# Performance work log

Hardware: AMD Instinct MI355X
Metric: run time of the kernel (lower is better)

## Reference

```python
import jax, jax.numpy as jnp
import numpy as np

EPS = 1e-12  # torch F.normalize eps


def _normalize(x):
    n = jnp.sqrt(jnp.sum(x * x, axis=1, keepdims=True))
    return x / jnp.maximum(n, EPS)


def _exp_sim(a, b, temp):
    # exp(a @ b.T / temp); returns (diag [B], row_sum [B,1])
    m = jnp.exp(jnp.matmul(a, b.T) / temp)
    return jnp.diagonal(m), jnp.sum(m, axis=1, keepdims=True)


def reference(x):
    temp = 0.1
    bsz = x.shape[0] // 3
    xn = _normalize(x)
    xe, ye, ze = xn[:bsz], xn[bsz:2 * bsz], xn[2 * bsz:]

    d_xx, s_xx = _exp_sim(xe, xe, temp)
    d_yy, s_yy = _exp_sim(ye, ye, temp)
    d_xy, s_xy = _exp_sim(xe, ye, temp)
    d_ax, s_ax = _exp_sim(xe, ze, temp)
    d_ay, s_ay = _exp_sim(ye, ze, temp)
    d_zx, s_zx = _exp_sim(ze, xe, temp)
    d_zy, s_zy = _exp_sim(ze, ye, temp)

    # NOTE: diag terms are [B], row-sums are [B,1] -> denominator broadcasts to
    # [B,B], matching the original torch broadcasting exactly.
    denom_mutual = (s_xy - d_xy) + (s_xx - d_xx) + (s_yy - d_yy)  # [B,B]
    loss_mutual = jnp.mean(-2.0 * jnp.log(d_xy / denom_mutual))

    def aux(d, s):
        return jnp.mean(-jnp.log(d / (s - d)))  # d/[B,B] -> [B,B]

    loss = (loss_mutual + aux(d_ax, s_ax) + aux(d_ay, s_ay)
            + aux(d_zx, s_zx) + aux(d_zy, s_zy))
    return loss


def setup_inputs() -> dict:
    key = jax.random.key(0)
    x = jax.random.normal(key, (12288, 128), dtype=jnp.float32)
    return {"x": x}
```

## Files before the change

### kernel.cpp

```cpp
#include <hip/hip_runtime.h>
#include <hip/hip_bf16.h>


typedef __attribute__((ext_vector_type(8))) short short8;
typedef __attribute__((ext_vector_type(4))) float floatx4;

#define D      128
#define BM     128
#define BN     64
#define BPAD   136
#define JSPLIT 32
#define NTPB   2
#define GRID_EXPSIM (5 * 32 * 32)

__global__ __launch_bounds__(256) void normalize_kernel(
    const float* __restrict__ x, short* __restrict__ xn,
    float* __restrict__ out, int rows) {
  int tid = threadIdx.x;
  if (blockIdx.x == 0 && tid == 0) out[0] = 0.0f;

  int row  = blockIdx.x * 4 + (tid >> 6);
  int lane = tid & 63;
  if (row >= rows) return;
  const float2* xr = (const float2*)(x + (size_t)row * D);
  float2 v = xr[lane];
  float s = v.x * v.x + v.y * v.y;
#pragma unroll
  for (int off = 1; off < 64; off <<= 1) s += __shfl_xor(s, off, 64);
  float scale = 3.7982825470322528f / fmaxf(sqrtf(s), 1e-12f);
  __hip_bfloat162 h;
  h.x = __float2bfloat16(v.x * scale);
  h.y = __float2bfloat16(v.y * scale);
  ((__hip_bfloat162*)xn)[(size_t)row * 64 + lane] = h;
}

template <bool COL, bool DIAG>
__device__ __forceinline__ void epilogue(
    const floatx4 (&acc)[2][4], float (&rs)[2][4], int rowg0, int colg0,
    int quad, int lm, int w, int t, float* __restrict__ csLDS,
    float* __restrict__ diag_ptr) {
  float cs[4] = {0.f, 0.f, 0.f, 0.f};
#pragma unroll
  for (int mi = 0; mi < 2; mi++) {
#pragma unroll
    for (int r = 0; r < 4; r++) {
      int rowg = rowg0 + mi * 16 + quad * 4 + r;
      float part = 0.f;
#pragma unroll
      for (int ni = 0; ni < 4; ni++) {
        float e = exp2f(acc[mi][ni][r]);
        part += e;
        if (COL) cs[ni] += e;
        if (DIAG) {
          if (colg0 + ni * 16 + lm == rowg) diag_ptr[rowg] = e;
        }
      }
      rs[mi][r] += part;
    }
  }
  if (COL) {
#pragma unroll
    for (int ni = 0; ni < 4; ni++) {
      float v = cs[ni];
      v += __shfl_xor(v, 16, 64);
      v += __shfl_xor(v, 32, 64);
      if (quad == 0) csLDS[w * 128 + t * 64 + ni * 16 + lm] = v;
    }
  }
}

__global__ __launch_bounds__(256) void expsim_kernel(
    const short* __restrict__ xn,
    float* __restrict__ srow,
    float* __restrict__ scol,
    float* __restrict__ diag,
    int bsz) {
  __shared__ short ldsB[BN * BPAD];
  __shared__ float csLDS[4 * 128];

  int tid = threadIdx.x;
  int bx  = blockIdx.x;
  int task   = bx >> 10;
  int rem    = bx & 1023;
  int iblk   = rem >> 5;
  int jsplit = rem & 31;

  const int aoff_t[5] = {0, 1, 0, 0, 1};
  const int boff_t[5] = {0, 1, 1, 2, 2};
  int arow0     = aoff_t[task] * bsz + iblk * BM;
  int brow_base = boff_t[task] * bsz;
  bool col_en   = (task >= 3);
  bool dg       = (jsplit == iblk);

  int w    = tid >> 6;
  int lane = tid & 63;
  int quad = lane >> 4;
  int lm   = lane & 15;
  int rowg0 = iblk * BM + w * 32;

  float* diag_ptr = diag + task * bsz;

  short8 afrag[2][4];
#pragma unroll
  for (int mi = 0; mi < 2; mi++) {
    int r = arow0 + w * 32 + mi * 16 + lm;
    const short8* ap = (const short8*)(xn + (size_t)r * D);
#pragma unroll
    for (int kk = 0; kk < 4; kk++) afrag[mi][kk] = ap[kk * 4 + quad];
  }

  float rs[2][4];
#pragma unroll
  for (int mi = 0; mi < 2; mi++)
#pragma unroll
    for (int r = 0; r < 4; r++) rs[mi][r] = 0.0f;

  const floatx4 z4 = {0.f, 0.f, 0.f, 0.f};

  for (int t = 0; t < NTPB; t++) {
    int jt    = jsplit * NTPB + t;
    int colg0 = jt * BN;
    __syncthreads();
    const short* bsrc = xn + ((size_t)brow_base + colg0) * D;
#pragma unroll
    for (int it = 0; it < 4; it++) {
      int c = it * 256 + tid;
      int br = c >> 4, c16 = c & 15;
      *(short8*)(&ldsB[br * BPAD + c16 * 8]) =
          *(const short8*)(bsrc + (size_t)br * D + c16 * 8);
    }
    __syncthreads();

    floatx4 acc[2][4];
#pragma unroll
    for (int kk = 0; kk < 4; kk++) {
      short8 bfrag[4];
#pragma unroll
      for (int ni = 0; ni < 4; ni++)
        bfrag[ni] = *(const short8*)(&ldsB[(ni * 16 + lm) * BPAD + kk * 32 + quad * 8]);
#pragma unroll
      for (int mi = 0; mi < 2; mi++)
#pragma unroll
        for (int ni = 0; ni < 4; ni++)
          acc[mi][ni] = __builtin_amdgcn_mfma_f32_16x16x32_bf16(
              afrag[mi][kk], bfrag[ni], (kk == 0) ? z4 : acc[mi][ni], 0, 0, 0);
    }

    if (col_en) {
      if (dg) epilogue<true, true>(acc, rs, rowg0, colg0, quad, lm, w, t, csLDS, diag_ptr);
      else    epilogue<true, false>(acc, rs, rowg0, colg0, quad, lm, w, t, csLDS, diag_ptr);
    } else {
      if (dg) epilogue<false, true>(acc, rs, rowg0, colg0, quad, lm, w, t, csLDS, diag_ptr);
      else    epilogue<false, false>(acc, rs, rowg0, colg0, quad, lm, w, t, csLDS, diag_ptr);
    }
  }

  float* srow_ptr = srow + ((size_t)(task * JSPLIT + jsplit)) * bsz;
#pragma unroll
  for (int mi = 0; mi < 2; mi++) {
#pragma unroll
    for (int r = 0; r < 4; r++) {
      float v = rs[mi][r];
      v += __shfl_xor(v, 1, 64);
      v += __shfl_xor(v, 2, 64);
      v += __shfl_xor(v, 4, 64);
      v += __shfl_xor(v, 8, 64);
      if (lm == 0) srow_ptr[rowg0 + mi * 16 + quad * 4 + r] = v;
    }
  }

  if (col_en) {
    __syncthreads();
    float* scol_ptr = scol + ((size_t)((task - 3) * 32 + iblk)) * bsz + jsplit * 128;
    if (tid < 128)
      scol_ptr[tid] = csLDS[tid] + csLDS[128 + tid] + csLDS[256 + tid] + csLDS[384 + tid];
  }
}

__global__ __launch_bounds__(256) void reduce_kernel(
    const float* __restrict__ srow, const float* __restrict__ scol,
    const float* __restrict__ diag, float* __restrict__ out, int bsz) {
  int tid = threadIdx.x;
  int i   = blockIdx.x * 256 + tid;

  float s[5];
#pragma unroll
  for (int t = 0; t < 5; t++) {
    float a = 0.f;
#pragma unroll 8
    for (int js = 0; js < JSPLIT; js++) a += srow[(size_t)(t * JSPLIT + js) * bsz + i];
    s[t] = a;
  }
  float s_zx = 0.f, s_zy = 0.f;
#pragma unroll 8
  for (int ib = 0; ib < 32; ib++) {
    s_zx += scol[(size_t)ib * bsz + i];
    s_zy += scol[(size_t)(32 + ib) * bsz + i];
  }
  float d_xx = diag[0 * bsz + i], d_yy = diag[1 * bsz + i];
  float d_xy = diag[2 * bsz + i], d_ax = diag[3 * bsz + i];
  float d_ay = diag[4 * bsz + i];

  float denom = (s[2] - d_xy) + (s[0] - d_xx) + (s[1] - d_yy);
  float tloc = -2.0f * __logf(d_xy / denom);
  tloc -= __logf(d_ax / (s[3] - d_ax));
  tloc -= __logf(d_ay / (s[4] - d_ay));
  tloc -= __logf(d_ax / (s_zx - d_ax));
  tloc -= __logf(d_ay / (s_zy - d_ay));

  __shared__ float red[256];
  red[tid] = tloc;
  __syncthreads();
  for (int st = 128; st > 0; st >>= 1) {
    if (tid < st) red[tid] += red[tid + st];
    __syncthreads();
  }
  if (tid == 0) atomicAdd(out, red[0] / (float)bsz);
}

extern "C" void kernel_launch(void* const* d_in, const int* in_sizes, int n_in,
                              void* d_out, int out_size, void* d_ws, size_t ws_size,
                              hipStream_t stream) {
  const float* x = (const float*)d_in[0];
  int rows = in_sizes[0] / D;
  int bsz  = rows / 3;

  char*  ws       = (char*)d_ws;
  short* xn       = (short*)ws;
  size_t xn_bytes = (size_t)rows * D * sizeof(short);
  float* srow     = (float*)(ws + xn_bytes);
  float* scol     = srow + 5 * JSPLIT * bsz;
  float* diag     = scol + 2 * 32 * bsz;

  normalize_kernel<<<rows / 4, 256, 0, stream>>>(x, xn, (float*)d_out, rows);
  expsim_kernel<<<GRID_EXPSIM, 256, 0, stream>>>(xn, srow, scol, diag, bsz);
  reduce_kernel<<<bsz / 256, 256, 0, stream>>>(srow, scol, diag, (float*)d_out, bsz);
}
```

Before: 116.4 us.

## Pre-swizzle normalized rows into MFMA fragment layout and drop LDS staging

The normalize kernel now writes bf16 rows in a fragment-major layout, so each lane's MFMA operand is one contiguous coalesced short8 load. The similarity kernel reads B fragments straight from global memory instead of staging them through LDS with syncthreads. Each block now covers 8 column tiles instead of 2, which gives a 4x smaller grid and fewer partial row-sum slices for the reduce kernel. The batch size is hard-coded to 4096, and the kernel now depends on L2 reuse of B fragments in place of LDS reuse.

```diff
diff --git a/kernel.cpp b/kernel.cpp
--- a/kernel.cpp
+++ b/kernel.cpp
@@ -5,16 +5,13 @@
 typedef __attribute__((ext_vector_type(8))) short short8;
 typedef __attribute__((ext_vector_type(4))) float floatx4;
 
-#define D      128
-#define BM     128
-#define BN     64
-#define BPAD   136
-#define JSPLIT 32
-#define NTPB   2
-#define GRID_EXPSIM (5 * 32 * 32)
+#define D   128
+#define BSZ 4096
+#define GPM 256
+#define GRID_EXPSIM (5 * 32 * 8)
 
 __global__ __launch_bounds__(256) void normalize_kernel(
-    const float* __restrict__ x, short* __restrict__ xn,
+    const float* __restrict__ x, __hip_bfloat162* __restrict__ xnf2,
     float* __restrict__ out, int rows) {
   int tid = threadIdx.x;
   if (blockIdx.x == 0 && tid == 0) out[0] = 0.0f;
@@ -31,15 +28,17 @@
   __hip_bfloat162 h;
   h.x = __float2bfloat16(v.x * scale);
   h.y = __float2bfloat16(v.y * scale);
-  ((__hip_bfloat162*)xn)[(size_t)row * 64 + lane] = h;
+  int g    = row >> 4;
+  int kk   = lane >> 4;
+  int quad = (lane >> 2) & 3;
+  int jj   = lane & 3;
+  xnf2[g * 1024 + kk * 256 + (quad * 16 + (row & 15)) * 4 + jj] = h;
 }
 
 template <bool COL, bool DIAG>
 __device__ __forceinline__ void epilogue(
-    const floatx4 (&acc)[2][4], float (&rs)[2][4], int rowg0, int colg0,
-    int quad, int lm, int w, int t, float* __restrict__ csLDS,
-    float* __restrict__ diag_ptr) {
-  float cs[4] = {0.f, 0.f, 0.f, 0.f};
+    const floatx4 (&acc)[2][4], float (&rs)[2][4], float (&cs)[4],
+    int rowg0, int colg0, int quad, int lm, float* __restrict__ diag_ptr) {
 #pragma unroll
   for (int mi = 0; mi < 2; mi++) {
 #pragma unroll
@@ -48,7 +47,7 @@
       float part = 0.f;
 #pragma unroll
       for (int ni = 0; ni < 4; ni++) {
-        float e = exp2f(acc[mi][ni][r]);
+        float e = __builtin_amdgcn_exp2f(acc[mi][ni][r]);
         part += e;
         if (COL) cs[ni] += e;
         if (DIAG) {
@@ -58,56 +57,44 @@
       rs[mi][r] += part;
     }
   }
-  if (COL) {
-#pragma unroll
-    for (int ni = 0; ni < 4; ni++) {
-      float v = cs[ni];
-      v += __shfl_xor(v, 16, 64);
-      v += __shfl_xor(v, 32, 64);
-      if (quad == 0) csLDS[w * 128 + t * 64 + ni * 16 + lm] = v;
-    }
-  }
 }
 
 __global__ __launch_bounds__(256) void expsim_kernel(
-    const short* __restrict__ xn,
+    const short8* __restrict__ xnf8,
     float* __restrict__ srow,
     float* __restrict__ scol,
-    float* __restrict__ diag,
-    int bsz) {
-  __shared__ short ldsB[BN * BPAD];
-  __shared__ float csLDS[4 * 128];
+    float* __restrict__ diag) {
+  __shared__ float csLDS[4 * 512];
 
   int tid = threadIdx.x;
   int bx  = blockIdx.x;
-  int task   = bx >> 10;
-  int rem    = bx & 1023;
-  int iblk   = rem >> 5;
-  int jsplit = rem & 31;
+  int task = bx >> 8;
+  int rem  = bx & 255;
+  int ib   = rem >> 3;
+  int jsp  = rem & 7;
 
   const int aoff_t[5] = {0, 1, 0, 0, 1};
   const int boff_t[5] = {0, 1, 1, 2, 2};
-  int arow0     = aoff_t[task] * bsz + iblk * BM;
-  int brow_base = boff_t[task] * bsz;
-  bool col_en   = (task >= 3);
-  bool dg       = (jsplit == iblk);
+  bool col_en = (task >= 3);
 
   int w    = tid >> 6;
   int lane = tid & 63;
   int quad = lane >> 4;
   int lm   = lane & 15;
-  int rowg0 = iblk * BM + w * 32;
-
-  float* diag_ptr = diag + task * bsz;
-
+  int rowg0 = ib * 128 + w * 32;
+
+  bool dgblk = (jsp == (ib >> 2));
+  int  tdiag = ((ib & 3) * 2) + (w >> 1);
+
+  float* diag_ptr = diag + task * BSZ;
+
+  int gA = aoff_t[task] * GPM + ib * 8 + w * 2;
   short8 afrag[2][4];
 #pragma unroll
-  for (int mi = 0; mi < 2; mi++) {
-    int r = arow0 + w * 32 + mi * 16 + lm;
-    const short8* ap = (const short8*)(xn + (size_t)r * D);
-#pragma unroll
-    for (int kk = 0; kk < 4; kk++) afrag[mi][kk] = ap[kk * 4 + quad];
-  }
+  for (int mi = 0; mi < 2; mi++)
+#pragma unroll
+    for (int kk = 0; kk < 4; kk++)
+      afrag[mi][kk] = xnf8[(size_t)(gA + mi) * 256 + kk * 64 + lane];
 
   float rs[2][4];
 #pragma unroll
@@ -116,46 +103,45 @@
     for (int r = 0; r < 4; r++) rs[mi][r] = 0.0f;
 
   const floatx4 z4 = {0.f, 0.f, 0.f, 0.f};
-
-  for (int t = 0; t < NTPB; t++) {
-    int jt    = jsplit * NTPB + t;
-    int colg0 = jt * BN;
-    __syncthreads();
-    const short* bsrc = xn + ((size_t)brow_base + colg0) * D;
-#pragma unroll
-    for (int it = 0; it < 4; it++) {
-      int c = it * 256 + tid;
-      int br = c >> 4, c16 = c & 15;
-      *(short8*)(&ldsB[br * BPAD + c16 * 8]) =
-          *(const short8*)(bsrc + (size_t)br * D + c16 * 8);
-    }
-    __syncthreads();
-
+  int gB0 = boff_t[task] * GPM + jsp * 32;
+
+#pragma unroll
+  for (int t = 0; t < 8; t++) {
+    int colg0 = (jsp * 8 + t) * 64;
     floatx4 acc[2][4];
 #pragma unroll
     for (int kk = 0; kk < 4; kk++) {
-      short8 bfrag[4];
+      short8 bf[4];
 #pragma unroll
       for (int ni = 0; ni < 4; ni++)
-        bfrag[ni] = *(const short8*)(&ldsB[(ni * 16 + lm) * BPAD + kk * 32 + quad * 8]);
+        bf[ni] = xnf8[(size_t)(gB0 + t * 4 + ni) * 256 + kk * 64 + lane];
 #pragma unroll
       for (int mi = 0; mi < 2; mi++)
 #pragma unroll
         for (int ni = 0; ni < 4; ni++)
           acc[mi][ni] = __builtin_amdgcn_mfma_f32_16x16x32_bf16(
-              afrag[mi][kk], bfrag[ni], (kk == 0) ? z4 : acc[mi][ni], 0, 0, 0);
-    }
-
+              afrag[mi][kk], bf[ni], (kk == 0) ? z4 : acc[mi][ni], 0, 0, 0);
+    }
+
+    float cs[4] = {0.f, 0.f, 0.f, 0.f};
+    bool dg = dgblk && (t == tdiag);
     if (col_en) {
-      if (dg) epilogue<true, true>(acc, rs, rowg0, colg0, quad, lm, w, t, csLDS, diag_ptr);
-      else    epilogue<true, false>(acc, rs, rowg0, colg0, quad, lm, w, t, csLDS, diag_ptr);
+      if (dg) epilogue<true, true>(acc, rs, cs, rowg0, colg0, quad, lm, diag_ptr);
+      else    epilogue<true, false>(acc, rs, cs, rowg0, colg0, quad, lm, diag_ptr);
+#pragma unroll
+      for (int ni = 0; ni < 4; ni++) {
+        float v = cs[ni];
+        v += __shfl_xor(v, 16, 64);
+        v += __shfl_xor(v, 32, 64);
+        if (quad == 0) csLDS[w * 512 + t * 64 + ni * 16 + lm] = v;
+      }
     } else {
-      if (dg) epilogue<false, true>(acc, rs, rowg0, colg0, quad, lm, w, t, csLDS, diag_ptr);
-      else    epilogue<false, false>(acc, rs, rowg0, colg0, quad, lm, w, t, csLDS, diag_ptr);
-    }
-  }
-
-  float* srow_ptr = srow + ((size_t)(task * JSPLIT + jsplit)) * bsz;
+      if (dg) epilogue<false, true>(acc, rs, cs, rowg0, colg0, quad, lm, diag_ptr);
+      else    epilogue<false, false>(acc, rs, cs, rowg0, colg0, quad, lm, diag_ptr);
+    }
+  }
+
+  float* srow_ptr = srow + ((size_t)(task * 8 + jsp)) * BSZ;
 #pragma unroll
   for (int mi = 0; mi < 2; mi++) {
 #pragma unroll
@@ -171,15 +157,15 @@
 
   if (col_en) {
     __syncthreads();
-    float* scol_ptr = scol + ((size_t)((task - 3) * 32 + iblk)) * bsz + jsplit * 128;
-    if (tid < 128)
-      scol_ptr[tid] = csLDS[tid] + csLDS[128 + tid] + csLDS[256 + tid] + csLDS[384 + tid];
+    float* scol_ptr = scol + ((size_t)((task - 3) * 32 + ib)) * BSZ + jsp * 512;
+    for (int c = tid; c < 512; c += 256)
+      scol_ptr[c] = csLDS[c] + csLDS[512 + c] + csLDS[1024 + c] + csLDS[1536 + c];
   }
 }
 
 __global__ __launch_bounds__(256) void reduce_kernel(
     const float* __restrict__ srow, const float* __restrict__ scol,
-    const float* __restrict__ diag, float* __restrict__ out, int bsz) {
+    const float* __restrict__ diag, float* __restrict__ out) {
   int tid = threadIdx.x;
   int i   = blockIdx.x * 256 + tid;
 
@@ -187,19 +173,19 @@
 #pragma unroll
   for (int t = 0; t < 5; t++) {
     float a = 0.f;
-#pragma unroll 8
-    for (int js = 0; js < JSPLIT; js++) a += srow[(size_t)(t * JSPLIT + js) * bsz + i];
+#pragma unroll
+    for (int js = 0; js < 8; js++) a += srow[(size_t)(t * 8 + js) * BSZ + i];
     s[t] = a;
   }
   float s_zx = 0.f, s_zy = 0.f;
 #pragma unroll 8
   for (int ib = 0; ib < 32; ib++) {
-    s_zx += scol[(size_t)ib * bsz + i];
-    s_zy += scol[(size_t)(32 + ib) * bsz + i];
-  }
-  float d_xx = diag[0 * bsz + i], d_yy = diag[1 * bsz + i];
-  float d_xy = diag[2 * bsz + i], d_ax = diag[3 * bsz + i];
-  float d_ay = diag[4 * bsz + i];
+    s_zx += scol[(size_t)ib * BSZ + i];
+    s_zy += scol[(size_t)(32 + ib) * BSZ + i];
+  }
+  float d_xx = diag[0 * BSZ + i], d_yy = diag[1 * BSZ + i];
+  float d_xy = diag[2 * BSZ + i], d_ax = diag[3 * BSZ + i];
+  float d_ay = diag[4 * BSZ + i];
 
   float denom = (s[2] - d_xy) + (s[0] - d_xx) + (s[1] - d_yy);
   float tloc = -2.0f * __logf(d_xy / denom);
@@ -215,7 +201,7 @@
     if (tid < st) red[tid] += red[tid + st];
     __syncthreads();
   }
-  if (tid == 0) atomicAdd(out, red[0] / (float)bsz);
+  if (tid == 0) atomicAdd(out, red[0] / (float)BSZ);
 }
 
 extern "C" void kernel_launch(void* const* d_in, const int* in_sizes, int n_in,
@@ -223,16 +209,17 @@
                               hipStream_t stream) {
   const float* x = (const float*)d_in[0];
   int rows = in_sizes[0] / D;
-  int bsz  = rows / 3;
 
   char*  ws       = (char*)d_ws;
-  short* xn       = (short*)ws;
+  short* xnf      = (short*)ws;
   size_t xn_bytes = (size_t)rows * D * sizeof(short);
   float* srow     = (float*)(ws + xn_bytes);
-  float* scol     = srow + 5 * JSPLIT * bsz;
-  float* diag     = scol + 2 * 32 * bsz;
-
-  normalize_kernel<<<rows / 4, 256, 0, stream>>>(x, xn, (float*)d_out, rows);
-  expsim_kernel<<<GRID_EXPSIM, 256, 0, stream>>>(xn, srow, scol, diag, bsz);
-  reduce_kernel<<<bsz / 256, 256, 0, stream>>>(srow, scol, diag, (float*)d_out, bsz);
-}
+  float* scol     = srow + 5 * 8 * BSZ;
+  float* diag     = scol + 2 * 32 * BSZ;
+
+  normalize_kernel<<<rows / 4, 256, 0, stream>>>(
+      x, (__hip_bfloat162*)xnf, (float*)d_out, rows);
+  expsim_kernel<<<GRID_EXPSIM, 256, 0, stream>>>(
+      (const short8*)xnf, srow, scol, diag);
+  reduce_kernel<<<16, 256, 0, stream>>>(srow, scol, diag, (float*)d_out);
+}
```

Measured after the change: 100.6 us. 13.6% less time.
